# Kernel tuning notes

Hardware: AMD Instinct MI355X
Metric: run time of the kernel (lower is better)

## Reference

```python
import jax, jax.numpy as jnp
import numpy as np

TEMPERATURE = 0.07
COS_EPS = 1e-8          # torch F.cosine_similarity eps
MASK_FILL = -9e15       # value used to mask the diagonal


def setup_inputs() -> dict:
    key = jax.random.key(0)
    k1, k2 = jax.random.split(key)
    B, D = 4096, 256
    z_i = jax.random.normal(k1, (B, D), dtype=jnp.float32)
    z_j = jax.random.normal(k2, (B, D), dtype=jnp.float32)
    return {"z_i": z_i, "z_j": z_j}


def reference(z_i, z_j):
    B = z_i.shape[0]
    z = jnp.concatenate([z_i, z_j], axis=0)                 # [2B, D]
    # cosine similarity = normalized-GEMM (same math as broadcasted version)
    norms = jnp.maximum(jnp.linalg.norm(z, axis=-1, keepdims=True), COS_EPS)
    zn = z / norms                                          # [2B, D]
    sim = zn @ zn.T                                         # [2B, 2B]
    # fused diagonal mask + temperature scale
    diag = jnp.eye(2 * B, dtype=bool)
    logits = jnp.where(diag, MASK_FILL, sim) / TEMPERATURE  # [2B, 2B]
    # positive pair labels: row k pairs with row (k+B) mod 2B
    labels = jnp.concatenate([jnp.arange(B, 2 * B), jnp.arange(0, B)])
    logp = jax.nn.log_softmax(logits, axis=-1)
    loss = -jnp.mean(jnp.take_along_axis(logp, labels[:, None], axis=-1))
    return loss
```

## Files before the change

kernel.cpp:

```cpp
#include <hip/hip_runtime.h>
#include <hip/hip_bf16.h>

#define B_ROWS 4096
#define TWOB   8192
#define DIM    256
#define INV_T  14.285714285714286f

#define BM 128
#define BN 128
#define NQ 8
#define NSLOT 80

typedef __bf16 bf16x8 __attribute__((ext_vector_type(8)));
typedef float  f32x4  __attribute__((ext_vector_type(4)));

__global__ __launch_bounds__(256) void normalize_k(const float* __restrict__ zi,
                                                   const float* __restrict__ zj,
                                                   unsigned short* __restrict__ zn,
                                                   float* __restrict__ loss_acc,
                                                   unsigned int* __restrict__ counter) {
    if (blockIdx.x == 0 && threadIdx.x == 0) {
        loss_acc[0] = 0.0f;
        counter[0]  = 0u;
    }
    int wave = threadIdx.x >> 6;
    int lane = threadIdx.x & 63;
    int row  = blockIdx.x * 4 + wave;
    const float* src = (row < B_ROWS) ? (zi + (size_t)row * DIM)
                                      : (zj + (size_t)(row - B_ROWS) * DIM);
    float4 v = reinterpret_cast<const float4*>(src)[lane];
    float ss = v.x * v.x + v.y * v.y + v.z * v.z + v.w * v.w;
#pragma unroll
    for (int off = 32; off >= 1; off >>= 1) ss += __shfl_xor(ss, off);
    float norm = sqrtf(ss);
    norm = fmaxf(norm, 1e-8f);
    float inv = 1.0f / norm;
    ushort4 o;
    o.x = __builtin_bit_cast(unsigned short, __float2bfloat16(v.x * inv));
    o.y = __builtin_bit_cast(unsigned short, __float2bfloat16(v.y * inv));
    o.z = __builtin_bit_cast(unsigned short, __float2bfloat16(v.z * inv));
    o.w = __builtin_bit_cast(unsigned short, __float2bfloat16(v.w * inv));
    reinterpret_cast<ushort4*>(zn)[(size_t)row * 64 + lane] = o;
}

__global__ __launch_bounds__(256) void ntxent_main(const unsigned short* __restrict__ znu,
                                                   float* __restrict__ pos,
                                                   float* __restrict__ strip_sums) {
    const __bf16* zn = (const __bf16*)znu;
    __shared__ __attribute__((aligned(16))) __bf16 As[8][BM * 32];
    __shared__ __attribute__((aligned(16))) __bf16 Bs[2][BN * 32];

    const int tid  = threadIdx.x;
    const int wave = tid >> 6;
    const int lane = tid & 63;
    const int wr = wave >> 1, wc = wave & 1;
    const int quad = lane >> 4, lc = lane & 15;
    const int rt = blockIdx.x;
    const int q  = blockIdx.y;
    const int q4 = q * 4;
    const int row0 = rt * BM;
    const int NCT = (q == 7 && rt < 32) ? 5 : 4;
#define COLOF(i) ((rt + (((i) == 4) ? 32 : (q4 + (i)))) & 63)

    int stg_off[2];
#pragma unroll
    for (int t = 0; t < 2; ++t) {
        int c  = (wave * 2 + t) * 64 + lane;
        int m  = c >> 2;
        int kc = (c & 3) ^ ((m & 3) ^ ((m >> 2) & 3));
        stg_off[t] = m * DIM + kc * 8;
    }

    const int sw    = (lc & 3) ^ ((lc >> 2) & 3);
    const int aBase = (wr * 64 + lc) * 64 + ((quad ^ sw) * 16);
    const int bBase = (wc * 64 + lc) * 64 + ((quad ^ sw) * 16);

#pragma unroll
    for (int kt = 0; kt < 8; ++kt) {
#pragma unroll
        for (int t = 0; t < 2; ++t) {
            const int j = wave * 2 + t;
            const __bf16* ga = zn + row0 * DIM + kt * 32 + stg_off[t];
            __builtin_amdgcn_global_load_lds(
                (const __attribute__((address_space(1))) void*)ga,
                (__attribute__((address_space(3))) void*)((char*)As + kt * 8192 + j * 1024), 16, 0, 0);
        }
    }
    {
        const int col0 = COLOF(0) * BN;
#pragma unroll
        for (int t = 0; t < 2; ++t) {
            const int j = wave * 2 + t;
            const __bf16* gb = zn + col0 * DIM + stg_off[t];
            __builtin_amdgcn_global_load_lds(
                (const __attribute__((address_space(1))) void*)gb,
                (__attribute__((address_space(3))) void*)((char*)Bs + j * 1024), 16, 0, 0);
        }
    }

    f32x4 acc[4][4];
    float rsum[4][4];
    float posv[4] = {0.f, 0.f, 0.f, 0.f};
    int   posm[4] = {-1, -1, -1, -1};
#pragma unroll
    for (int mi = 0; mi < 4; ++mi)
#pragma unroll
        for (int r = 0; r < 4; ++r) rsum[mi][r] = 0.0f;

    for (int ct = 0; ct < NCT; ++ct) {
        const int jdist = (ct == 4) ? 32 : (q4 + ct);
        const int c     = (rt + jdist) & 63;
        const int col0  = c * BN;
#pragma unroll
        for (int mi = 0; mi < 4; ++mi)
#pragma unroll
            for (int ni = 0; ni < 4; ++ni) acc[mi][ni] = f32x4{0.f, 0.f, 0.f, 0.f};

#pragma unroll
        for (int kt = 0; kt < 8; ++kt) {
            __syncthreads();

            {
                const int nct = (kt == 7) ? ct + 1 : ct;
                const int nkt = (kt + 1) & 7;
                if (nct < NCT) {
                    const int ncol0 = COLOF(nct) * BN;
#pragma unroll
                    for (int t = 0; t < 2; ++t) {
                        const int j = wave * 2 + t;
                        const __bf16* gb = zn + ncol0 * DIM + nkt * 32 + stg_off[t];
                        __builtin_amdgcn_global_load_lds(
                            (const __attribute__((address_space(1))) void*)gb,
                            (__attribute__((address_space(3))) void*)((char*)Bs + ((kt + 1) & 1) * 8192 + j * 1024),
                            16, 0, 0);
                    }
                }
            }

            bf16x8 af[4], bfr[4];
#pragma unroll
            for (int mi = 0; mi < 4; ++mi)
                af[mi] = *(const bf16x8*)((const char*)As + kt * 8192 + aBase + mi * 1024);
#pragma unroll
            for (int ni = 0; ni < 4; ++ni)
                bfr[ni] = *(const bf16x8*)((const char*)Bs + (kt & 1) * 8192 + bBase + ni * 1024);
#pragma unroll
            for (int mi = 0; mi < 4; ++mi)
#pragma unroll
                for (int ni = 0; ni < 4; ++ni)
                    acc[mi][ni] = __builtin_amdgcn_mfma_f32_16x16x32_bf16(
                        af[mi], bfr[ni], acc[mi][ni], 0, 0, 0);
        }

        const bool isDiag = (jdist == 0);
        const bool isPos  = (jdist == 32);
        float cadd[4] = {0.f, 0.f, 0.f, 0.f};
#pragma unroll
        for (int mi = 0; mi < 4; ++mi) {
#pragma unroll
            for (int ni = 0; ni < 4; ++ni) {
                f32x4 a = acc[mi][ni];
#pragma unroll
                for (int r = 0; r < 4; ++r) {
                    float logit = a[r] * INV_T;
                    float e = __expf(logit);
                    if (isDiag || isPos) {
                        int gr = row0 + wr * 64 + mi * 16 + quad * 4 + r;
                        int gc = col0 + wc * 64 + ni * 16 + lc;
                        if (isPos && gc == gr + B_ROWS) { posv[mi] = logit; posm[mi] = gr; }
                        if (isDiag && gr == gc) e = 0.0f;
                    }
                    rsum[mi][r] += e;
                    cadd[ni]    += e;
                }
            }
        }

        if (!isDiag) {
#pragma unroll
            for (int ni = 0; ni < 4; ++ni) {
                cadd[ni] += __shfl_xor(cadd[ni], 16);
                cadd[ni] += __shfl_xor(cadd[ni], 32);
            }
            if (quad == 0) {
                float* dst = strip_sums + (size_t)((jdist - 1) * 2 + wr) * TWOB + col0 + wc * 64 + lc;
#pragma unroll
                for (int ni = 0; ni < 4; ++ni) dst[ni * 16] = cadd[ni];
            }
        }
    }

#pragma unroll
    for (int mi = 0; mi < 4; ++mi)
        if (posm[mi] >= 0) {
            pos[posm[mi]] = posv[mi];
            pos[posm[mi] + B_ROWS] = posv[mi];
        }

    {
        float* rdst = strip_sums + (size_t)(64 + q * 2 + wc) * TWOB + row0 + wr * 64;
#pragma unroll
        for (int mi = 0; mi < 4; ++mi) {
#pragma unroll
            for (int r = 0; r < 4; ++r) {
                float v = rsum[mi][r];
                v += __shfl_xor(v, 1);
                v += __shfl_xor(v, 2);
                v += __shfl_xor(v, 4);
                v += __shfl_xor(v, 8);
                if (lc == 0) rdst[mi * 16 + quad * 4 + r] = v;
            }
        }
    }
}

__global__ __launch_bounds__(256) void finalize_k(const float* __restrict__ strip_sums,
                                                  const float* __restrict__ pos,
                                                  float* __restrict__ loss_acc,
                                                  unsigned int* __restrict__ counter,
                                                  float* __restrict__ out) {
    __shared__ float wsums[4];
    const int tid = threadIdx.x;
    const int r   = blockIdx.x * 256 + tid;
    float s = 0.0f;
#pragma unroll
    for (int t = 0; t < 62; ++t) s += strip_sums[(size_t)t * TWOB + r];
    if (r >= B_ROWS) {
        s += strip_sums[(size_t)62 * TWOB + r];
        s += strip_sums[(size_t)63 * TWOB + r];
    }
#pragma unroll
    for (int t = 64; t < 80; ++t) s += strip_sums[(size_t)t * TWOB + r];
    float local = logf(s) - pos[r];
#pragma unroll
    for (int off = 32; off >= 1; off >>= 1) local += __shfl_xor(local, off);
    if ((tid & 63) == 0) wsums[tid >> 6] = local;
    __syncthreads();
    if (tid == 0) {
        float bsum = wsums[0] + wsums[1] + wsums[2] + wsums[3];
        atomicAdd(loss_acc, bsum);
        __threadfence();
        unsigned int done = atomicAdd(counter, 1u);
        if (done == gridDim.x - 1) {
            float total = atomicAdd(loss_acc, 0.0f);
            out[0] = total / (float)TWOB;
        }
    }
}

extern "C" void kernel_launch(void* const* d_in, const int* in_sizes, int n_in,
                              void* d_out, int out_size, void* d_ws, size_t ws_size,
                              hipStream_t stream) {
    const float* zi = (const float*)d_in[0];
    const float* zj = (const float*)d_in[1];
    unsigned short* zn = (unsigned short*)d_ws;
    float* pos        = (float*)((char*)d_ws + (size_t)TWOB * DIM * 2);
    float* strip_sums = pos + TWOB;
    float* loss_acc   = strip_sums + (size_t)NSLOT * TWOB;
    unsigned int* counter = (unsigned int*)(loss_acc + 1);
    float* out = (float*)d_out;

    normalize_k<<<dim3(TWOB / 4), 256, 0, stream>>>(zi, zj, zn, loss_acc, counter);
    ntxent_main<<<dim3(64, NQ), 256, 0, stream>>>(zn, pos, strip_sums);
    finalize_k<<<dim3(TWOB / 256), 256, 0, stream>>>(strip_sums, pos, loss_acc, counter, out);
}
```

Baseline: 99.10 us.

## Deepen B-tile pipeline, double-buffer fragments, and halve grid y-dimension

The B operand buffer grows from a 2-stage to a 4-stage LDS ring with prefetch distance 3. It uses explicit vmcnt/lgkmcnt waits and raw s_barrier instead of __syncthreads. Register fragments are double-buffered and MFMA runs at raised priority to overlap LDS reads with compute. The grid's y-dimension drops from 8 to 4, so each block processes 8 or 9 column tiles, the A-tile load is amortized over more tiles, and the finalize kernel sums fewer strip slots. The cost is lower block count and occupancy (launch_bounds 256,1 and more LDS), plus hand-tuned wait counts that could be fragile.

```diff
diff --git a/kernel.cpp b/kernel.cpp
--- a/kernel.cpp
+++ b/kernel.cpp
@@ -8,8 +8,8 @@
 
 #define BM 128
 #define BN 128
-#define NQ 8
-#define NSLOT 80
+#define NQ 4
+#define NSLOT 72
 
 typedef __bf16 bf16x8 __attribute__((ext_vector_type(8)));
 typedef float  f32x4  __attribute__((ext_vector_type(4)));
@@ -43,12 +43,12 @@
     reinterpret_cast<ushort4*>(zn)[(size_t)row * 64 + lane] = o;
 }
 
-__global__ __launch_bounds__(256) void ntxent_main(const unsigned short* __restrict__ znu,
-                                                   float* __restrict__ pos,
-                                                   float* __restrict__ strip_sums) {
+__global__ __launch_bounds__(256, 1) void ntxent_main(const unsigned short* __restrict__ znu,
+                                                      float* __restrict__ pos,
+                                                      float* __restrict__ strip_sums) {
     const __bf16* zn = (const __bf16*)znu;
     __shared__ __attribute__((aligned(16))) __bf16 As[8][BM * 32];
-    __shared__ __attribute__((aligned(16))) __bf16 Bs[2][BN * 32];
+    __shared__ __attribute__((aligned(16))) __bf16 Bs[4][BN * 32];
 
     const int tid  = threadIdx.x;
     const int wave = tid >> 6;
@@ -57,10 +57,8 @@
     const int quad = lane >> 4, lc = lane & 15;
     const int rt = blockIdx.x;
     const int q  = blockIdx.y;
-    const int q4 = q * 4;
     const int row0 = rt * BM;
-    const int NCT = (q == 7 && rt < 32) ? 5 : 4;
-#define COLOF(i) ((rt + (((i) == 4) ? 32 : (q4 + (i)))) & 63)
+    const int NCT = (q == 3 && rt < 32) ? 9 : 8;
 
     int stg_off[2];
 #pragma unroll
@@ -74,6 +72,19 @@
     const int sw    = (lc & 3) ^ ((lc >> 2) & 3);
     const int aBase = (wr * 64 + lc) * 64 + ((quad ^ sw) * 16);
     const int bBase = (wc * 64 + lc) * 64 + ((quad ^ sw) * 16);
+
+#define STAGEC(C_) do { \
+        const int tC_ = (C_) >> 3; \
+        const int jd_ = (tC_ == 8) ? 32 : (q * 8 + tC_); \
+        const int c0_ = ((rt + jd_) & 63) * BN; \
+        _Pragma("unroll") \
+        for (int t_ = 0; t_ < 2; ++t_) { \
+            const int j_ = wave * 2 + t_; \
+            const __bf16* gb_ = zn + c0_ * DIM + ((C_) & 7) * 32 + stg_off[t_]; \
+            __builtin_amdgcn_global_load_lds( \
+                (const __attribute__((address_space(1))) void*)gb_, \
+                (__attribute__((address_space(3))) void*)((char*)Bs + ((C_) & 3) * 8192 + j_ * 1024), 16, 0, 0); \
+        } } while (0)
 
 #pragma unroll
     for (int kt = 0; kt < 8; ++kt) {
@@ -86,19 +97,10 @@
                 (__attribute__((address_space(3))) void*)((char*)As + kt * 8192 + j * 1024), 16, 0, 0);
         }
     }
-    {
-        const int col0 = COLOF(0) * BN;
-#pragma unroll
-        for (int t = 0; t < 2; ++t) {
-            const int j = wave * 2 + t;
-            const __bf16* gb = zn + col0 * DIM + stg_off[t];
-            __builtin_amdgcn_global_load_lds(
-                (const __attribute__((address_space(1))) void*)gb,
-                (__attribute__((address_space(3))) void*)((char*)Bs + j * 1024), 16, 0, 0);
-        }
-    }
+    STAGEC(0); STAGEC(1); STAGEC(2);
 
     f32x4 acc[4][4];
+    bf16x8 afr[2][4], bfr[2][4];
     float rsum[4][4];
     float posv[4] = {0.f, 0.f, 0.f, 0.f};
     int   posm[4] = {-1, -1, -1, -1};
@@ -107,50 +109,52 @@
 #pragma unroll
         for (int r = 0; r < 4; ++r) rsum[mi][r] = 0.0f;
 
+    asm volatile("s_waitcnt vmcnt(4)" ::: "memory");
+    __builtin_amdgcn_s_barrier();
+    __builtin_amdgcn_sched_barrier(0);
+#pragma unroll
+    for (int mi = 0; mi < 4; ++mi)
+        afr[0][mi] = *(const bf16x8*)((const char*)As + aBase + mi * 1024);
+#pragma unroll
+    for (int ni = 0; ni < 4; ++ni)
+        bfr[0][ni] = *(const bf16x8*)((const char*)Bs + bBase + ni * 1024);
+
+#define KSTEP(KT) do { \
+        if (ct == NCT - 1 && (KT) >= 5) { asm volatile("s_waitcnt vmcnt(0)" ::: "memory"); } \
+        else                            { asm volatile("s_waitcnt vmcnt(2)" ::: "memory"); } \
+        __builtin_amdgcn_s_barrier(); \
+        __builtin_amdgcn_sched_barrier(0); \
+        { const int C_ = ct * 8 + (KT) + 3; \
+          if ((C_ >> 3) < NCT) STAGEC(C_); } \
+        _Pragma("unroll") \
+        for (int mi = 0; mi < 4; ++mi) \
+            afr[((KT) + 1) & 1][mi] = *(const bf16x8*)((const char*)As + (((KT) + 1) & 7) * 8192 + aBase + mi * 1024); \
+        _Pragma("unroll") \
+        for (int ni = 0; ni < 4; ++ni) \
+            bfr[((KT) + 1) & 1][ni] = *(const bf16x8*)((const char*)Bs + (((KT) + 1) & 3) * 8192 + bBase + ni * 1024); \
+        asm volatile("s_waitcnt lgkmcnt(8)" ::: "memory"); \
+        __builtin_amdgcn_sched_barrier(0); \
+        __builtin_amdgcn_s_setprio(1); \
+        _Pragma("unroll") \
+        for (int mi = 0; mi < 4; ++mi) \
+            _Pragma("unroll") \
+            for (int ni = 0; ni < 4; ++ni) \
+                acc[mi][ni] = __builtin_amdgcn_mfma_f32_16x16x32_bf16( \
+                    afr[(KT) & 1][mi], bfr[(KT) & 1][ni], acc[mi][ni], 0, 0, 0); \
+        __builtin_amdgcn_s_setprio(0); \
+    } while (0)
+
+#pragma unroll 1
     for (int ct = 0; ct < NCT; ++ct) {
-        const int jdist = (ct == 4) ? 32 : (q4 + ct);
-        const int c     = (rt + jdist) & 63;
-        const int col0  = c * BN;
+        const int jdist = (ct == 8) ? 32 : (q * 8 + ct);
+        const int col0  = ((rt + jdist) & 63) * BN;
 #pragma unroll
         for (int mi = 0; mi < 4; ++mi)
 #pragma unroll
             for (int ni = 0; ni < 4; ++ni) acc[mi][ni] = f32x4{0.f, 0.f, 0.f, 0.f};
 
-#pragma unroll
-        for (int kt = 0; kt < 8; ++kt) {
-            __syncthreads();
-
-            {
-                const int nct = (kt == 7) ? ct + 1 : ct;
-                const int nkt = (kt + 1) & 7;
-                if (nct < NCT) {
-                    const int ncol0 = COLOF(nct) * BN;
-#pragma unroll
-                    for (int t = 0; t < 2; ++t) {
-                        const int j = wave * 2 + t;
-                        const __bf16* gb = zn + ncol0 * DIM + nkt * 32 + stg_off[t];
-                        __builtin_amdgcn_global_load_lds(
-                            (const __attribute__((address_space(1))) void*)gb,
-                            (__attribute__((address_space(3))) void*)((char*)Bs + ((kt + 1) & 1) * 8192 + j * 1024),
-                            16, 0, 0);
-                    }
-                }
-            }
-
-            bf16x8 af[4], bfr[4];
-#pragma unroll
-            for (int mi = 0; mi < 4; ++mi)
-                af[mi] = *(const bf16x8*)((const char*)As + kt * 8192 + aBase + mi * 1024);
-#pragma unroll
-            for (int ni = 0; ni < 4; ++ni)
-                bfr[ni] = *(const bf16x8*)((const char*)Bs + (kt & 1) * 8192 + bBase + ni * 1024);
-#pragma unroll
-            for (int mi = 0; mi < 4; ++mi)
-#pragma unroll
-                for (int ni = 0; ni < 4; ++ni)
-                    acc[mi][ni] = __builtin_amdgcn_mfma_f32_16x16x32_bf16(
-                        af[mi], bfr[ni], acc[mi][ni], 0, 0, 0);
-        }
+        KSTEP(0); KSTEP(1); KSTEP(2); KSTEP(3);
+        KSTEP(4); KSTEP(5); KSTEP(6); KSTEP(7);
 
         const bool isDiag = (jdist == 0);
         const bool isPos  = (jdist == 32);
@@ -230,7 +234,7 @@
         s += strip_sums[(size_t)63 * TWOB + r];
     }
 #pragma unroll
-    for (int t = 64; t < 80; ++t) s += strip_sums[(size_t)t * TWOB + r];
+    for (int t = 64; t < 72; ++t) s += strip_sums[(size_t)t * TWOB + r];
     float local = logf(s) - pos[r];
 #pragma unroll
     for (int off = 32; off >= 1; off >>= 1) local += __shfl_xor(local, off);
```

Measured after the change: 111.4 us. 12.4% more time.
